# Kernel optimization log

Measured on AMD Instinct MI355X. Metric: run time of the kernel, lower is better.

Reference implementation:

```python
import jax, jax.numpy as jnp
import numpy as np

N_NODES = 100000
N_EDGES = 1600000
IN_FEA, HIDDEN, RANK = 128, 128, 64


def setup_inputs() -> dict:
    key = jax.random.key(0)
    ks = jax.random.split(key, 6)
    stdv = 1.0 / np.sqrt(HIDDEN)  # reset_parameters uses 1/sqrt(V.size(0)) = 1/sqrt(hidden)
    return {
        "x": jax.random.normal(ks[0], (N_NODES, IN_FEA), dtype=jnp.float32),
        "norm": jax.random.uniform(ks[1], (N_NODES, 1), dtype=jnp.float32),
        "W": jax.random.uniform(ks[2], (IN_FEA, RANK), minval=-stdv, maxval=stdv, dtype=jnp.float32),
        "V": jax.random.uniform(ks[3], (HIDDEN, RANK), minval=-stdv, maxval=stdv, dtype=jnp.float32),
        "src": jax.random.randint(ks[4], (N_EDGES,), 0, N_NODES, dtype=jnp.int32),
        "dst": jax.random.randint(ks[5], (N_EDGES,), 0, N_NODES, dtype=jnp.int32),
    }


def _segment_prod(m, seg, num_segments):
    # product-reduce over ragged mailboxes via sign/log decomposition
    # (numerically equivalent to prod, differentiable: d prod / d m_i = prod / m_i)
    logp = jax.ops.segment_sum(jnp.log(jnp.abs(m)), seg, num_segments=num_segments)
    n_neg = jax.ops.segment_sum((m < 0).astype(m.dtype), seg, num_segments=num_segments)
    sign = 1.0 - 2.0 * jnp.mod(n_neg, 2.0)
    # nodes with no in-edges get logp=0, sign=1 -> product identity 1
    return sign * jnp.exp(logp)


def reference(x, norm, W, V, src, dst):
    n = x.shape[0]
    h = x @ W                      # [N, rank] linear projection
    m = h[src]                     # [E, rank] gather messages along edges
    neigh = _segment_prod(m, dst, n)   # [N, rank] elementwise-product aggregation
    trans_x = norm * neigh         # [N, rank]
    return trans_x @ V.T           # [N, hidden]
```

## Files before the change

### kernel.cpp

```cpp
#include <hip/hip_runtime.h>
#include <hip/hip_bf16.h>

#define N_NODES 100000
#define N_EDGES 1600000
#define IN_FEA 128
#define HIDDEN 128
#define RANK 64

#define NBUCK 391
#define C_BLOCKS 1024
#define EPB 1563
#define S_BLOCKS 256
#define CHUNK_W (EPB * 4)
#define GEMM1_BLOCKS 1563

#define NPW 2
#define AGG_BLOCKS 3125


__device__ __forceinline__ void fma4(float4& a, float s, const float4& b) {
    a.x = fmaf(s, b.x, a.x);
    a.y = fmaf(s, b.y, a.y);
    a.z = fmaf(s, b.z, a.z);
    a.w = fmaf(s, b.w, a.w);
}

__device__ __forceinline__ unsigned short f2bf_rne(float f) {
    unsigned u = __float_as_uint(f);
    u += 0x7fffu + ((u >> 16) & 1u);
    return (unsigned short)(u >> 16);
}

__device__ __forceinline__ float bfu_lo(unsigned u) {
    return __uint_as_float(u << 16);
}
__device__ __forceinline__ float bfu_hi(unsigned u) {
    return __uint_as_float(u & 0xffff0000u);
}


__global__ __launch_bounds__(256) void gemm1_hist_kernel(const float* __restrict__ x,
                                                         const float* __restrict__ W,
                                                         unsigned short* __restrict__ hb,
                                                         const int* __restrict__ dst,
                                                         int* __restrict__ bhist,
                                                         int* __restrict__ blockhist) {
    __shared__ float Wl[IN_FEA * RANK];
    int t = threadIdx.x;

    if (blockIdx.x >= GEMM1_BLOCKS) {
        int* hist = (int*)Wl;
        int b = blockIdx.x - GEMM1_BLOCKS;
        for (int i = t; i < NBUCK; i += 256) hist[i] = 0;
        __syncthreads();
        int b0 = b * EPB;
        int b1 = min(b0 + EPB, N_EDGES);
        for (int e = b0 + t; e < b1; e += 256)
            atomicAdd(&hist[dst[e] >> 8], 1);
        __syncthreads();
        for (int i = t; i < NBUCK; i += 256) {
            int c = hist[i];
            blockhist[b * NBUCK + i] = c;
            if (c) atomicAdd(&bhist[i], c);
        }
        return;
    }

    for (int i = t; i < IN_FEA * RANK; i += 256) Wl[i] = W[i];
    __syncthreads();

    int r0 = (t & 15) * 4;
    int n0 = blockIdx.x * 64 + (t >> 4) * 4;
    const float4* x0 = (const float4*)(x + (long)min(n0 + 0, N_NODES - 1) * IN_FEA);
    const float4* x1 = (const float4*)(x + (long)min(n0 + 1, N_NODES - 1) * IN_FEA);
    const float4* x2 = (const float4*)(x + (long)min(n0 + 2, N_NODES - 1) * IN_FEA);
    const float4* x3 = (const float4*)(x + (long)min(n0 + 3, N_NODES - 1) * IN_FEA);
    float4 a0 = {0.f, 0.f, 0.f, 0.f}, a1 = a0, a2 = a0, a3 = a0;
    for (int k4 = 0; k4 < IN_FEA / 4; ++k4) {
        float4 v0 = x0[k4], v1 = x1[k4], v2 = x2[k4], v3 = x3[k4];
        int kb = k4 * 4;
        float4 w0 = *(const float4*)&Wl[(kb + 0) * RANK + r0];
        float4 w1 = *(const float4*)&Wl[(kb + 1) * RANK + r0];
        float4 w2 = *(const float4*)&Wl[(kb + 2) * RANK + r0];
        float4 w3 = *(const float4*)&Wl[(kb + 3) * RANK + r0];
        fma4(a0, v0.x, w0); fma4(a0, v0.y, w1); fma4(a0, v0.z, w2); fma4(a0, v0.w, w3);
        fma4(a1, v1.x, w0); fma4(a1, v1.y, w1); fma4(a1, v1.z, w2); fma4(a1, v1.w, w3);
        fma4(a2, v2.x, w0); fma4(a2, v2.y, w1); fma4(a2, v2.z, w2); fma4(a2, v2.w, w3);
        fma4(a3, v3.x, w0); fma4(a3, v3.y, w1); fma4(a3, v3.z, w2); fma4(a3, v3.w, w3);
    }
    float4 accs[4] = {a0, a1, a2, a3};
#pragma unroll
    for (int i = 0; i < 4; ++i) {
        if (n0 + i < N_NODES) {
            ushort4 o;
            o.x = f2bf_rne(accs[i].x); o.y = f2bf_rne(accs[i].y);
            o.z = f2bf_rne(accs[i].z); o.w = f2bf_rne(accs[i].w);
            *(ushort4*)(hb + (n0 + i) * RANK + r0) = o;
        }
    }
}


__global__ void bucket_scan_kernel(const int* __restrict__ bhist,
                                   int* __restrict__ bucket_offs,
                                   int* __restrict__ bucket_cursor,
                                   int* __restrict__ offs) {
    __shared__ int sd[512];
    int t = threadIdx.x;
    int v = (t < NBUCK) ? bhist[t] : 0;
    sd[t] = v;
    __syncthreads();
    for (int off = 1; off < 512; off <<= 1) {
        int a = 0;
        if (t >= off) a = sd[t - off];
        __syncthreads();
        sd[t] += a;
        __syncthreads();
    }
    if (t < NBUCK) {
        int excl = sd[t] - v;
        bucket_offs[t] = excl;
        bucket_cursor[t] = excl;
    }
    if (t == 0) {
        bucket_offs[NBUCK] = N_EDGES;
        offs[N_NODES] = N_EDGES;
    }
}

__global__ __launch_bounds__(1024) void binscatter_kernel(const int* __restrict__ src,
                                                          const int* __restrict__ dst,
                                                          const int* __restrict__ blockhist,
                                                          int* __restrict__ bucket_cursor,
                                                          unsigned* __restrict__ pairs) {
    __shared__ int wbase[NBUCK];
    __shared__ int cur[NBUCK];
    int t = threadIdx.x;
    int b = blockIdx.x;
    if (t < NBUCK) {
        int s = 0;
#pragma unroll
        for (int k = 0; k < 4; ++k)
            s += blockhist[(4 * b + k) * NBUCK + t];
        wbase[t] = s ? atomicAdd(&bucket_cursor[t], s) : 0;
        cur[t] = 0;
    }
    __syncthreads();
    int e0 = b * CHUNK_W;
    int e1 = min(e0 + CHUNK_W, N_EDGES);
    for (int e = e0 + t; e < e1; e += 1024) {
        int d = dst[e];
        int s = src[e];
        int bk = d >> 8;
        int lp = atomicAdd(&cur[bk], 1);
        pairs[wbase[bk] + lp] = ((unsigned)s << 8) | (unsigned)(d & 255);
    }
}

__global__ __launch_bounds__(1024) void bucket_build_kernel(const unsigned* __restrict__ pairs,
                                                            const int* __restrict__ bucket_offs,
                                                            int* __restrict__ offs,
                                                            int* __restrict__ eidx) {
    __shared__ int dcnt[256];
    __shared__ int sd[256];
    __shared__ int cur[256];
    int b = blockIdx.x, t = threadIdx.x;
    int base = bucket_offs[b], end = bucket_offs[b + 1];
    if (t < 256) dcnt[t] = 0;
    __syncthreads();
    for (int i = base + t; i < end; i += 1024)
        atomicAdd(&dcnt[pairs[i] & 255u], 1);
    __syncthreads();
    int v = 0;
    if (t < 256) { v = dcnt[t]; sd[t] = v; }
    __syncthreads();
    for (int off = 1; off < 256; off <<= 1) {
        int a = 0;
        if (t >= off && t < 256) a = sd[t - off];
        __syncthreads();
        if (t < 256) sd[t] += a;
        __syncthreads();
    }
    if (t < 256) {
        int excl = sd[t] - v;
        int node = b * 256 + t;
        if (node < N_NODES) offs[node] = base + excl;
        cur[t] = excl;
    }
    __syncthreads();
    for (int i = base + t; i < end; i += 1024) {
        unsigned r = pairs[i];
        int lp = atomicAdd(&cur[r & 255u], 1);
        eidx[base + lp] = (int)(r >> 8);
    }
}


__global__ __launch_bounds__(1024) void agg_gemm_kernel(const unsigned short* __restrict__ hb,
                                                        const float* __restrict__ norm,
                                                        const float* __restrict__ V,
                                                        const int* __restrict__ offs,
                                                        const int* __restrict__ eidx,
                                                        float* __restrict__ out) {
    __shared__ float VL[HIDDEN * 68];
    __shared__ float pls[16][NPW][64];
    int t = threadIdx.x;
    {
        const float4* V4 = (const float4*)V;
#pragma unroll
        for (int k = 0; k < 2; ++k) {
            int i4 = t + 1024 * k;
            float4 v = V4[i4];
            int el = i4 << 2;
            *(float4*)&VL[(el >> 6) * 68 + (el & 63)] = v;
        }
    }
    __syncthreads();

    int wave = t >> 6, lane = t & 63;
    int half = lane >> 5;
    int l32 = lane & 31;
    int nb = (blockIdx.x * 16 + wave) * NPW;
    const unsigned* hb2 = (const unsigned*)hb;

#pragma unroll
    for (int i = 0; i < NPW; ++i) {
        int node = nb + i;
        int beg = offs[node], end = offs[node + 1];

        float plo = 1.0f, phi = 1.0f;
        for (int c = beg; c < end; c += 64) {
            int n = min(64, end - c);
            int sidx = (c + lane < end) ? eidx[c + lane] : 0;
            int j = 0;
            for (; j + 16 <= n; j += 16) {
                int s0 = __shfl(sidx, j + 0  + half);
                int s1 = __shfl(sidx, j + 2  + half);
                int s2 = __shfl(sidx, j + 4  + half);
                int s3 = __shfl(sidx, j + 6  + half);
                int s4 = __shfl(sidx, j + 8  + half);
                int s5 = __shfl(sidx, j + 10 + half);
                int s6 = __shfl(sidx, j + 12 + half);
                int s7 = __shfl(sidx, j + 14 + half);
                unsigned u0 = hb2[(s0 << 5) | l32];
                unsigned u1 = hb2[(s1 << 5) | l32];
                unsigned u2 = hb2[(s2 << 5) | l32];
                unsigned u3 = hb2[(s3 << 5) | l32];
                unsigned u4 = hb2[(s4 << 5) | l32];
                unsigned u5 = hb2[(s5 << 5) | l32];
                unsigned u6 = hb2[(s6 << 5) | l32];
                unsigned u7 = hb2[(s7 << 5) | l32];
                plo *= ((bfu_lo(u0) * bfu_lo(u1)) * (bfu_lo(u2) * bfu_lo(u3))) *
                       ((bfu_lo(u4) * bfu_lo(u5)) * (bfu_lo(u6) * bfu_lo(u7)));
                phi *= ((bfu_hi(u0) * bfu_hi(u1)) * (bfu_hi(u2) * bfu_hi(u3))) *
                       ((bfu_hi(u4) * bfu_hi(u5)) * (bfu_hi(u6) * bfu_hi(u7)));
            }
            for (; j + 8 <= n; j += 8) {
                int s0 = __shfl(sidx, j + 0 + half);
                int s1 = __shfl(sidx, j + 2 + half);
                int s2 = __shfl(sidx, j + 4 + half);
                int s3 = __shfl(sidx, j + 6 + half);
                unsigned u0 = hb2[(s0 << 5) | l32];
                unsigned u1 = hb2[(s1 << 5) | l32];
                unsigned u2 = hb2[(s2 << 5) | l32];
                unsigned u3 = hb2[(s3 << 5) | l32];
                plo *= (bfu_lo(u0) * bfu_lo(u1)) * (bfu_lo(u2) * bfu_lo(u3));
                phi *= (bfu_hi(u0) * bfu_hi(u1)) * (bfu_hi(u2) * bfu_hi(u3));
            }
            for (; j < n; j += 2) {
                int jj = j + half;
                int s = __shfl(sidx, jj);
                unsigned u = hb2[(s << 5) | l32];
                float alo = bfu_lo(u), ahi = bfu_hi(u);
                if (jj >= n) { alo = 1.0f; ahi = 1.0f; }
                plo *= alo;
                phi *= ahi;
            }
        }
        plo *= __shfl_xor(plo, 32);
        phi *= __shfl_xor(phi, 32);

        if (lane < 32) {
            float nrm = norm[node];
            float2 o;
            o.x = plo * nrm;
            o.y = phi * nrm;
            *(float2*)&pls[wave][i][l32 * 2] = o;
        }
    }

    const float4* rA = (const float4*)&VL[lane * 68];
    const float4* rB = (const float4*)&VL[(lane + 64) * 68];
    const float4* p0 = (const float4*)pls[wave][0];
    const float4* p1 = (const float4*)pls[wave][1];
    float aA0 = 0.f, aB0 = 0.f, aA1 = 0.f, aB1 = 0.f;
#pragma unroll
    for (int q = 0; q < 16; ++q) {
        float4 va = rA[q];
        float4 vb = rB[q];
        float4 pp;
        pp = p0[q];
        aA0 = fmaf(pp.x, va.x, fmaf(pp.y, va.y, fmaf(pp.z, va.z, fmaf(pp.w, va.w, aA0))));
        aB0 = fmaf(pp.x, vb.x, fmaf(pp.y, vb.y, fmaf(pp.z, vb.z, fmaf(pp.w, vb.w, aB0))));
        pp = p1[q];
        aA1 = fmaf(pp.x, va.x, fmaf(pp.y, va.y, fmaf(pp.z, va.z, fmaf(pp.w, va.w, aA1))));
        aB1 = fmaf(pp.x, vb.x, fmaf(pp.y, vb.y, fmaf(pp.z, vb.z, fmaf(pp.w, vb.w, aB1))));
    }
    out[(nb + 0) * HIDDEN + lane]      = aA0;
    out[(nb + 0) * HIDDEN + 64 + lane] = aB0;
    out[(nb + 1) * HIDDEN + lane]      = aA1;
    out[(nb + 1) * HIDDEN + 64 + lane] = aB1;
}


extern "C" void kernel_launch(void* const* d_in, const int* in_sizes, int n_in,
                              void* d_out, int out_size, void* d_ws, size_t ws_size,
                              hipStream_t stream) {
    const float* x    = (const float*)d_in[0];
    const float* norm = (const float*)d_in[1];
    const float* W    = (const float*)d_in[2];
    const float* V    = (const float*)d_in[3];
    const int*   src  = (const int*)d_in[4];
    const int*   dst  = (const int*)d_in[5];
    float* out = (float*)d_out;

    unsigned short* hb = (unsigned short*)d_ws;
    int*   offs        = (int*)(hb + (long)N_NODES * RANK);
    int*   eidx        = offs + N_NODES + 1;
    int*   bhist       = eidx + N_EDGES;
    int*   bucket_offs = bhist + NBUCK;
    int*   bucket_cur  = bucket_offs + NBUCK + 1;

    unsigned* pairs    = (unsigned*)d_out;
    int*     blockhist = (int*)d_out + 2097152;

    hipMemsetAsync(bhist, 0, NBUCK * sizeof(int), stream);
    gemm1_hist_kernel<<<GEMM1_BLOCKS + C_BLOCKS, 256, 0, stream>>>(x, W, hb, dst, bhist, blockhist);
    bucket_scan_kernel<<<1, 512, 0, stream>>>(bhist, bucket_offs, bucket_cur, offs);
    binscatter_kernel<<<S_BLOCKS, 1024, 0, stream>>>(src, dst, blockhist, bucket_cur, pairs);
    bucket_build_kernel<<<NBUCK, 1024, 0, stream>>>(pairs, bucket_offs, offs, eidx);
    agg_gemm_kernel<<<AGG_BLOCKS, 1024, 0, stream>>>(hb, norm, V, offs, eidx, out);
}
```

Measured before the change: 246.0 us.

## Fuse per-node CSR build into aggregation kernel using LDS edge lists

```diff
diff --git a/kernel.cpp b/kernel.cpp
--- a/kernel.cpp
+++ b/kernel.cpp
@@ -14,8 +14,8 @@
 #define CHUNK_W (EPB * 4)
 #define GEMM1_BLOCKS 1563
 
-#define NPW 2
-#define AGG_BLOCKS 3125
+#define AGG_BLOCKS 782
+#define CAPE 4096
 
 
 __device__ __forceinline__ void fma4(float4& a, float s, const float4& b) {
@@ -103,8 +103,7 @@
 
 __global__ void bucket_scan_kernel(const int* __restrict__ bhist,
                                    int* __restrict__ bucket_offs,
-                                   int* __restrict__ bucket_cursor,
-                                   int* __restrict__ offs) {
+                                   int* __restrict__ bucket_cursor) {
     __shared__ int sd[512];
     int t = threadIdx.x;
     int v = (t < NBUCK) ? bhist[t] : 0;
@@ -122,10 +121,7 @@
         bucket_offs[t] = excl;
         bucket_cursor[t] = excl;
     }
-    if (t == 0) {
-        bucket_offs[NBUCK] = N_EDGES;
-        offs[N_NODES] = N_EDGES;
-    }
+    if (t == 0) bucket_offs[NBUCK] = N_EDGES;
 }
 
 __global__ __launch_bounds__(1024) void binscatter_kernel(const int* __restrict__ src,
@@ -157,53 +153,19 @@
     }
 }
 
-__global__ __launch_bounds__(1024) void bucket_build_kernel(const unsigned* __restrict__ pairs,
-                                                            const int* __restrict__ bucket_offs,
-                                                            int* __restrict__ offs,
-                                                            int* __restrict__ eidx) {
-    __shared__ int dcnt[256];
-    __shared__ int sd[256];
-    __shared__ int cur[256];
-    int b = blockIdx.x, t = threadIdx.x;
-    int base = bucket_offs[b], end = bucket_offs[b + 1];
-    if (t < 256) dcnt[t] = 0;
-    __syncthreads();
-    for (int i = base + t; i < end; i += 1024)
-        atomicAdd(&dcnt[pairs[i] & 255u], 1);
-    __syncthreads();
-    int v = 0;
-    if (t < 256) { v = dcnt[t]; sd[t] = v; }
-    __syncthreads();
-    for (int off = 1; off < 256; off <<= 1) {
-        int a = 0;
-        if (t >= off && t < 256) a = sd[t - off];
-        __syncthreads();
-        if (t < 256) sd[t] += a;
-        __syncthreads();
-    }
-    if (t < 256) {
-        int excl = sd[t] - v;
-        int node = b * 256 + t;
-        if (node < N_NODES) offs[node] = base + excl;
-        cur[t] = excl;
-    }
-    __syncthreads();
-    for (int i = base + t; i < end; i += 1024) {
-        unsigned r = pairs[i];
-        int lp = atomicAdd(&cur[r & 255u], 1);
-        eidx[base + lp] = (int)(r >> 8);
-    }
-}
-
 
 __global__ __launch_bounds__(1024) void agg_gemm_kernel(const unsigned short* __restrict__ hb,
                                                         const float* __restrict__ norm,
                                                         const float* __restrict__ V,
-                                                        const int* __restrict__ offs,
-                                                        const int* __restrict__ eidx,
+                                                        const unsigned* __restrict__ pairs,
+                                                        const int* __restrict__ bucket_offs,
                                                         float* __restrict__ out) {
     __shared__ float VL[HIDDEN * 68];
-    __shared__ float pls[16][NPW][64];
+    __shared__ float pls[16][2][64];
+    __shared__ int eidx_lds[CAPE];
+    __shared__ int dcnt[128];
+    __shared__ int sdv[128];
+    __shared__ int curv[128];
     int t = threadIdx.x;
     {
         const float4* V4 = (const float4*)V;
@@ -215,101 +177,143 @@
             *(float4*)&VL[(el >> 6) * 68 + (el & 63)] = v;
         }
     }
+    int bkt = blockIdx.x >> 1;
+    unsigned halfb = blockIdx.x & 1;
+    int e0 = bucket_offs[bkt], e1 = bucket_offs[bkt + 1];
+    if (t < 128) dcnt[t] = 0;
+    __syncthreads();
+
+    for (int i = e0 + t; i < e1; i += 1024) {
+        unsigned r = pairs[i];
+        if (((r >> 7) & 1u) == halfb) atomicAdd(&dcnt[r & 127u], 1);
+    }
+    __syncthreads();
+
+    int v = 0;
+    if (t < 128) { v = dcnt[t]; sdv[t] = v; }
+    __syncthreads();
+    for (int off = 1; off < 128; off <<= 1) {
+        int a = 0;
+        if (t >= off && t < 128) a = sdv[t - off];
+        __syncthreads();
+        if (t < 128) sdv[t] += a;
+        __syncthreads();
+    }
+    if (t < 128) curv[t] = sdv[t] - v;
+    __syncthreads();
+
+    for (int i = e0 + t; i < e1; i += 1024) {
+        unsigned r = pairs[i];
+        if (((r >> 7) & 1u) == halfb) {
+            int lp = atomicAdd(&curv[r & 127u], 1);
+            if (lp < CAPE) eidx_lds[lp] = (int)(r >> 8);
+        }
+    }
     __syncthreads();
 
     int wave = t >> 6, lane = t & 63;
     int half = lane >> 5;
     int l32 = lane & 31;
-    int nb = (blockIdx.x * 16 + wave) * NPW;
+    int nbase = blockIdx.x * 128;
     const unsigned* hb2 = (const unsigned*)hb;
 
-#pragma unroll
-    for (int i = 0; i < NPW; ++i) {
-        int node = nb + i;
-        int beg = offs[node], end = offs[node + 1];
-
-        float plo = 1.0f, phi = 1.0f;
-        for (int c = beg; c < end; c += 64) {
-            int n = min(64, end - c);
-            int sidx = (c + lane < end) ? eidx[c + lane] : 0;
-            int j = 0;
-            for (; j + 16 <= n; j += 16) {
-                int s0 = __shfl(sidx, j + 0  + half);
-                int s1 = __shfl(sidx, j + 2  + half);
-                int s2 = __shfl(sidx, j + 4  + half);
-                int s3 = __shfl(sidx, j + 6  + half);
-                int s4 = __shfl(sidx, j + 8  + half);
-                int s5 = __shfl(sidx, j + 10 + half);
-                int s6 = __shfl(sidx, j + 12 + half);
-                int s7 = __shfl(sidx, j + 14 + half);
-                unsigned u0 = hb2[(s0 << 5) | l32];
-                unsigned u1 = hb2[(s1 << 5) | l32];
-                unsigned u2 = hb2[(s2 << 5) | l32];
-                unsigned u3 = hb2[(s3 << 5) | l32];
-                unsigned u4 = hb2[(s4 << 5) | l32];
-                unsigned u5 = hb2[(s5 << 5) | l32];
-                unsigned u6 = hb2[(s6 << 5) | l32];
-                unsigned u7 = hb2[(s7 << 5) | l32];
-                plo *= ((bfu_lo(u0) * bfu_lo(u1)) * (bfu_lo(u2) * bfu_lo(u3))) *
-                       ((bfu_lo(u4) * bfu_lo(u5)) * (bfu_lo(u6) * bfu_lo(u7)));
-                phi *= ((bfu_hi(u0) * bfu_hi(u1)) * (bfu_hi(u2) * bfu_hi(u3))) *
-                       ((bfu_hi(u4) * bfu_hi(u5)) * (bfu_hi(u6) * bfu_hi(u7)));
+#pragma clang loop unroll(disable)
+    for (int rp = 0; rp < 4; ++rp) {
+#pragma unroll
+        for (int i = 0; i < 2; ++i) {
+            int ln = wave * 8 + rp * 2 + i;
+            int node = nbase + ln;
+            int beg = sdv[ln] - dcnt[ln];
+            int end = sdv[ln];
+
+            float plo = 1.0f, phi = 1.0f;
+            for (int c = beg; c < end; c += 64) {
+                int n = min(64, end - c);
+                int sidx = (c + lane < end) ? eidx_lds[c + lane] : 0;
+                int j = 0;
+                for (; j + 16 <= n; j += 16) {
+                    int s0 = __shfl(sidx, j + 0  + half);
+                    int s1 = __shfl(sidx, j + 2  + half);
+                    int s2 = __shfl(sidx, j + 4  + half);
+                    int s3 = __shfl(sidx, j + 6  + half);
+                    int s4 = __shfl(sidx, j + 8  + half);
+                    int s5 = __shfl(sidx, j + 10 + half);
+                    int s6 = __shfl(sidx, j + 12 + half);
+                    int s7 = __shfl(sidx, j + 14 + half);
+                    unsigned u0 = hb2[(s0 << 5) | l32];
+                    unsigned u1 = hb2[(s1 << 5) | l32];
+                    unsigned u2 = hb2[(s2 << 5) | l32];
+                    unsigned u3 = hb2[(s3 << 5) | l32];
+                    unsigned u4 = hb2[(s4 << 5) | l32];
+                    unsigned u5 = hb2[(s5 << 5) | l32];
+                    unsigned u6 = hb2[(s6 << 5) | l32];
+                    unsigned u7 = hb2[(s7 << 5) | l32];
+                    plo *= ((bfu_lo(u0) * bfu_lo(u1)) * (bfu_lo(u2) * bfu_lo(u3))) *
+                           ((bfu_lo(u4) * bfu_lo(u5)) * (bfu_lo(u6) * bfu_lo(u7)));
+                    phi *= ((bfu_hi(u0) * bfu_hi(u1)) * (bfu_hi(u2) * bfu_hi(u3))) *
+                           ((bfu_hi(u4) * bfu_hi(u5)) * (bfu_hi(u6) * bfu_hi(u7)));
+                }
+                for (; j + 8 <= n; j += 8) {
+                    int s0 = __shfl(sidx, j + 0 + half);
+                    int s1 = __shfl(sidx, j + 2 + half);
+                    int s2 = __shfl(sidx, j + 4 + half);
+                    int s3 = __shfl(sidx, j + 6 + half);
+                    unsigned u0 = hb2[(s0 << 5) | l32];
+                    unsigned u1 = hb2[(s1 << 5) | l32];
+                    unsigned u2 = hb2[(s2 << 5) | l32];
+                    unsigned u3 = hb2[(s3 << 5) | l32];
+                    plo *= (bfu_lo(u0) * bfu_lo(u1)) * (bfu_lo(u2) * bfu_lo(u3));
+                    phi *= (bfu_hi(u0) * bfu_hi(u1)) * (bfu_hi(u2) * bfu_hi(u3));
+                }
+                for (; j < n; j += 2) {
+                    int jj = j + half;
+                    int s = __shfl(sidx, jj);
+                    unsigned u = hb2[(s << 5) | l32];
+                    float alo = bfu_lo(u), ahi = bfu_hi(u);
+                    if (jj >= n) { alo = 1.0f; ahi = 1.0f; }
+                    plo *= alo;
+                    phi *= ahi;
+                }
             }
-            for (; j + 8 <= n; j += 8) {
-                int s0 = __shfl(sidx, j + 0 + half);
-                int s1 = __shfl(sidx, j + 2 + half);
-                int s2 = __shfl(sidx, j + 4 + half);
-                int s3 = __shfl(sidx, j + 6 + half);
-                unsigned u0 = hb2[(s0 << 5) | l32];
-                unsigned u1 = hb2[(s1 << 5) | l32];
-                unsigned u2 = hb2[(s2 << 5) | l32];
-                unsigned u3 = hb2[(s3 << 5) | l32];
-                plo *= (bfu_lo(u0) * bfu_lo(u1)) * (bfu_lo(u2) * bfu_lo(u3));
-                phi *= (bfu_hi(u0) * bfu_hi(u1)) * (bfu_hi(u2) * bfu_hi(u3));
+            plo *= __shfl_xor(plo, 32);
+            phi *= __shfl_xor(phi, 32);
+
+            if (lane < 32) {
+                float nrm = (node < N_NODES) ? norm[node] : 0.f;
+                float2 o;
+                o.x = plo * nrm;
+                o.y = phi * nrm;
+                *(float2*)&pls[wave][i][l32 * 2] = o;
             }
-            for (; j < n; j += 2) {
-                int jj = j + half;
-                int s = __shfl(sidx, jj);
-                unsigned u = hb2[(s << 5) | l32];
-                float alo = bfu_lo(u), ahi = bfu_hi(u);
-                if (jj >= n) { alo = 1.0f; ahi = 1.0f; }
-                plo *= alo;
-                phi *= ahi;
-            }
-        }
-        plo *= __shfl_xor(plo, 32);
-        phi *= __shfl_xor(phi, 32);
-
-        if (lane < 32) {
-            float nrm = norm[node];
-            float2 o;
-            o.x = plo * nrm;
-            o.y = phi * nrm;
-            *(float2*)&pls[wave][i][l32 * 2] = o;
-        }
-    }
-
-    const float4* rA = (const float4*)&VL[lane * 68];
-    const float4* rB = (const float4*)&VL[(lane + 64) * 68];
-    const float4* p0 = (const float4*)pls[wave][0];
-    const float4* p1 = (const float4*)pls[wave][1];
-    float aA0 = 0.f, aB0 = 0.f, aA1 = 0.f, aB1 = 0.f;
-#pragma unroll
-    for (int q = 0; q < 16; ++q) {
-        float4 va = rA[q];
-        float4 vb = rB[q];
-        float4 pp;
-        pp = p0[q];
-        aA0 = fmaf(pp.x, va.x, fmaf(pp.y, va.y, fmaf(pp.z, va.z, fmaf(pp.w, va.w, aA0))));
-        aB0 = fmaf(pp.x, vb.x, fmaf(pp.y, vb.y, fmaf(pp.z, vb.z, fmaf(pp.w, vb.w, aB0))));
-        pp = p1[q];
-        aA1 = fmaf(pp.x, va.x, fmaf(pp.y, va.y, fmaf(pp.z, va.z, fmaf(pp.w, va.w, aA1))));
-        aB1 = fmaf(pp.x, vb.x, fmaf(pp.y, vb.y, fmaf(pp.z, vb.z, fmaf(pp.w, vb.w, aB1))));
-    }
-    out[(nb + 0) * HIDDEN + lane]      = aA0;
-    out[(nb + 0) * HIDDEN + 64 + lane] = aB0;
-    out[(nb + 1) * HIDDEN + lane]      = aA1;
-    out[(nb + 1) * HIDDEN + 64 + lane] = aB1;
+        }
+
+        int n0 = nbase + wave * 8 + rp * 2;
+        const float4* rA = (const float4*)&VL[lane * 68];
+        const float4* rB = (const float4*)&VL[(lane + 64) * 68];
+        const float4* p0 = (const float4*)pls[wave][0];
+        const float4* p1 = (const float4*)pls[wave][1];
+        float aA0 = 0.f, aB0 = 0.f, aA1 = 0.f, aB1 = 0.f;
+#pragma unroll
+        for (int q = 0; q < 16; ++q) {
+            float4 va = rA[q];
+            float4 vb = rB[q];
+            float4 pp;
+            pp = p0[q];
+            aA0 = fmaf(pp.x, va.x, fmaf(pp.y, va.y, fmaf(pp.z, va.z, fmaf(pp.w, va.w, aA0))));
+            aB0 = fmaf(pp.x, vb.x, fmaf(pp.y, vb.y, fmaf(pp.z, vb.z, fmaf(pp.w, vb.w, aB0))));
+            pp = p1[q];
+            aA1 = fmaf(pp.x, va.x, fmaf(pp.y, va.y, fmaf(pp.z, va.z, fmaf(pp.w, va.w, aA1))));
+            aB1 = fmaf(pp.x, vb.x, fmaf(pp.y, vb.y, fmaf(pp.z, vb.z, fmaf(pp.w, vb.w, aB1))));
+        }
+        if (n0 < N_NODES) {
+            out[n0 * HIDDEN + lane]      = aA0;
+            out[n0 * HIDDEN + 64 + lane] = aB0;
+        }
+        if (n0 + 1 < N_NODES) {
+            out[(n0 + 1) * HIDDEN + lane]      = aA1;
+            out[(n0 + 1) * HIDDEN + 64 + lane] = aB1;
+        }
+    }
 }
 
 
@@ -325,19 +329,16 @@
     float* out = (float*)d_out;
 
     unsigned short* hb = (unsigned short*)d_ws;
-    int*   offs        = (int*)(hb + (long)N_NODES * RANK);
-    int*   eidx        = offs + N_NODES + 1;
-    int*   bhist       = eidx + N_EDGES;
+    unsigned* pairs    = (unsigned*)(hb + (long)N_NODES * RANK);
+    int*   bhist       = (int*)(pairs + N_EDGES);
     int*   bucket_offs = bhist + NBUCK;
     int*   bucket_cur  = bucket_offs + NBUCK + 1;
 
-    unsigned* pairs    = (unsigned*)d_out;
-    int*     blockhist = (int*)d_out + 2097152;
+    int* blockhist = (int*)d_out + 2097152;
 
     hipMemsetAsync(bhist, 0, NBUCK * sizeof(int), stream);
     gemm1_hist_kernel<<<GEMM1_BLOCKS + C_BLOCKS, 256, 0, stream>>>(x, W, hb, dst, bhist, blockhist);
-    bucket_scan_kernel<<<1, 512, 0, stream>>>(bhist, bucket_offs, bucket_cur, offs);
+    bucket_scan_kernel<<<1, 512, 0, stream>>>(bhist, bucket_offs, bucket_cur);
     binscatter_kernel<<<S_BLOCKS, 1024, 0, stream>>>(src, dst, blockhist, bucket_cur, pairs);
-    bucket_build_kernel<<<NBUCK, 1024, 0, stream>>>(pairs, bucket_offs, offs, eidx);
-    agg_gemm_kernel<<<AGG_BLOCKS, 1024, 0, stream>>>(hb, norm, V, offs, eidx, out);
-}
+    agg_gemm_kernel<<<AGG_BLOCKS, 1024, 0, stream>>>(hb, norm, V, pairs, bucket_offs, out);
+}
```

Result: slower. 663.3 us (+169.6%).
